# Optimization experiments

Measured on AMD Instinct MI355X. Metric: run time of the kernel, lower is better.

The kernel has to match this reference:

```python
import jax, jax.numpy as jnp
import numpy as np

IN_CH, D, K = 256, 128, 512

def setup_inputs() -> dict:
    key = jax.random.key(0)
    k1, k2, k3, k4 = jax.random.split(key, 4)
    x = jax.random.normal(k1, (16, IN_CH, 64, 64), dtype=jnp.float32)
    W = jax.random.normal(k2, (D, IN_CH), dtype=jnp.float32) * (1.0 / np.sqrt(IN_CH))
    b = jax.random.normal(k3, (D,), dtype=jnp.float32) * 0.01
    prototypes = jax.random.normal(k4, (K, D), dtype=jnp.float32) * 0.02
    gamma = jnp.asarray(1.0, dtype=jnp.float32)
    return {"x": x, "W": W, "b": b, "prototypes": prototypes, "gamma": gamma}

def reference(x, W, b, prototypes, gamma):
    n, c, h, w = x.shape
    # 1x1 conv projection: [n,c,h,w] -> [n,h,w,d]
    q = jnp.einsum('nchw,dc->nhwd', x, W) + b
    q_flat = q.reshape(n * h * w, -1)                      # [T, d]
    q_norm2 = jnp.sum(q_flat * q_flat, axis=1, keepdims=True)   # [T, 1]
    p_norm2 = jnp.sum(prototypes * prototypes, axis=1)[None, :] # [1, K]
    dist2 = q_norm2 + p_norm2 - 2.0 * (q_flat @ prototypes.T)   # [T, K]
    weights = jax.nn.softmax(-jnp.abs(gamma) * dist2, axis=1)
    return weights.reshape(n, h, w, -1).transpose(0, 3, 1, 2)   # [n, K, h, w]
```

## Files before the change

kernel.cpp:

```cpp
#include <hip/hip_runtime.h>

#define HW 4096
#define NCH 256
#define DIM 128
#define NPROTO 512

typedef __attribute__((ext_vector_type(4))) float f32x4;
typedef __attribute__((ext_vector_type(8))) short s16x8;
typedef __attribute__((ext_vector_type(4))) short s16x4;
typedef __attribute__((ext_vector_type(2))) unsigned u32x2;

__device__ __forceinline__ unsigned short f2bf(float f) {
  union { float f; unsigned u; } v; v.f = f;
  unsigned r = v.u + 0x7fffu + ((v.u >> 16) & 1u);
  return (unsigned short)(r >> 16);
}

__global__ __launch_bounds__(256) void prep_kernel(const float* __restrict__ P,
                                                   const float* __restrict__ Wm,
                                                   unsigned short* __restrict__ Pr,
                                                   unsigned short* __restrict__ Wr,
                                                   float* __restrict__ pn2) {
  const int tid = threadIdx.x;
  if (blockIdx.x < 8) {
    const int n  = blockIdx.x * 64 + (tid >> 2);
    const int qt = tid & 3;
    const float* row = P + n * DIM + qt * 32;
    unsigned short* dst = Pr + ((size_t)qt * NPROTO + n) * 32;
    float ssq = 0.f;
#pragma unroll
    for (int u = 0; u < 8; ++u) {
      f32x4 v = *(const f32x4*)(row + 4 * u);
      ssq += v.x * v.x + v.y * v.y + v.z * v.z + v.w * v.w;
      dst[4 * u + 0] = f2bf(v.x);
      dst[4 * u + 1] = f2bf(v.y);
      dst[4 * u + 2] = f2bf(v.z);
      dst[4 * u + 3] = f2bf(v.w);
    }
    ssq += __shfl_xor(ssq, 1);
    ssq += __shfl_xor(ssq, 2);
    if (qt == 0) pn2[n] = ssq;
  } else {
#pragma unroll
    for (int it = 0; it < 2; ++it) {
      const int p  = (blockIdx.x - 8) * 256 + tid + 512 * it;
      const int d  = p >> 3;
      const int ch = p & 7;
      const float* src = Wm + d * NCH + 32 * ch;
      unsigned short* dst = Wr + ((size_t)ch * DIM + d) * 32;
#pragma unroll
      for (int u = 0; u < 8; ++u) {
        f32x4 v = *(const f32x4*)(src + 4 * u);
        dst[4 * u + 0] = f2bf(v.x);
        dst[4 * u + 1] = f2bf(v.y);
        dst[4 * u + 2] = f2bf(v.z);
        dst[4 * u + 3] = f2bf(v.w);
      }
    }
  }
}

__global__ __launch_bounds__(512) void fused_kernel(const float* __restrict__ x,
                                                    const unsigned short* __restrict__ Wr,
                                                    const float* __restrict__ bias,
                                                    const unsigned short* __restrict__ Pr,
                                                    const float* __restrict__ pn2,
                                                    const float* __restrict__ gptr,
                                                    float* __restrict__ out) {
  __shared__ __align__(16) char smem[25088];
  unsigned short* x_s = (unsigned short*)smem;
  unsigned short* q_s = (unsigned short*)(smem + 16384);
  float* red  = (float*)smem;
  float* rmx  = (float*)smem + 256;
  float* rinv = (float*)smem + 288;

  const int tid  = threadIdx.x;
  const int p0   = blockIdx.x * 32;
  const int nimg = p0 >> 12;
  const int hw0  = p0 & 4095;
  const int wave = tid >> 6, lane = tid & 63;
  const int l15 = lane & 15, l4 = lane >> 4;
  const float g = fabsf(gptr[0]);

  {
    const int f  = tid & 7;
    const int gg = (tid >> 3) & 31;
    const int h  = tid >> 8;
    const float* src = x + (size_t)nimg * NCH * HW + hw0
                         + (size_t)(8 * gg + 4 * h) * HW + 4 * f;
    f32x4 v0 = *(const f32x4*)(src);
    f32x4 v1 = *(const f32x4*)(src + HW);
    f32x4 v2 = *(const f32x4*)(src + 2 * HW);
    f32x4 v3 = *(const f32x4*)(src + 3 * HW);
#pragma unroll
    for (int j = 0; j < 4; ++j) {
      const int pix  = 4 * f + j;
      const int slot = (gg & 24) | ((gg ^ (pix >> 1)) & 7);
      u32x2 wv;
      wv.x = (unsigned)f2bf(v0[j]) | ((unsigned)f2bf(v1[j]) << 16);
      wv.y = (unsigned)f2bf(v2[j]) | ((unsigned)f2bf(v3[j]) << 16);
      *(u32x2*)(x_s + pix * 256 + slot * 8 + 4 * h) = wv;
    }
  }
  __syncthreads();

  {
    const int mtb  = (wave & 3) * 2;
    const int nt   = wave >> 2;
    const int pixb = 16 * nt + l15;
    f32x4 qa0 = {0.f, 0.f, 0.f, 0.f};
    f32x4 qa1 = {0.f, 0.f, 0.f, 0.f};
#pragma unroll
    for (int kc = 0; kc < 8; ++kc) {
      const int gb   = 4 * kc + l4;
      const int slot = (gb & 24) | ((gb ^ (pixb >> 1)) & 7);
      s16x8 xb = *(const s16x8*)(x_s + pixb * 256 + slot * 8);
      const unsigned short* wb = Wr + (size_t)(kc * DIM + l15) * 32 + 8 * l4;
      s16x8 w0 = *(const s16x8*)(wb + (size_t)(16 * mtb) * 32);
      s16x8 w1 = *(const s16x8*)(wb + (size_t)(16 * (mtb + 1)) * 32);
      qa0 = __builtin_amdgcn_mfma_f32_16x16x32_bf16(w0, xb, qa0, 0, 0, 0);
      qa1 = __builtin_amdgcn_mfma_f32_16x16x32_bf16(w1, xb, qa1, 0, 0, 0);
    }
#pragma unroll
    for (int mm = 0; mm < 2; ++mm) {
      const int d0 = 16 * (mtb + mm) + 4 * l4;
      f32x4 qa = mm ? qa1 : qa0;
      f32x4 bv = *(const f32x4*)(bias + d0);
      s16x4 o;
#pragma unroll
      for (int r = 0; r < 4; ++r) o[r] = (short)f2bf(qa[r] + bv[r]);
      *(s16x4*)(q_s + pixb * 136 + d0) = o;
    }
  }
  __syncthreads();

  f32x4 acc[2][4];
#pragma unroll
  for (int i = 0; i < 2; ++i)
#pragma unroll
    for (int j = 0; j < 4; ++j)
#pragma unroll
      for (int r = 0; r < 4; ++r) acc[i][j][r] = 0.f;

#pragma unroll
  for (int kc = 0; kc < 4; ++kc) {
    s16x8 afr[2];
#pragma unroll
    for (int i = 0; i < 2; ++i)
      afr[i] = *(const s16x8*)(q_s + (16 * i + l15) * 136 + 32 * kc + 8 * l4);
    const unsigned short* pb = Pr + (size_t)(kc * NPROTO + 64 * wave + l15) * 32 + 8 * l4;
#pragma unroll
    for (int j = 0; j < 4; ++j) {
      s16x8 bfr = *(const s16x8*)(pb + (size_t)(16 * j) * 32);
#pragma unroll
      for (int i = 0; i < 2; ++i)
        acc[i][j] = __builtin_amdgcn_mfma_f32_16x16x32_bf16(afr[i], bfr, acc[i][j], 0, 0, 0);
    }
  }

  float pnv[4];
#pragma unroll
  for (int j = 0; j < 4; ++j) pnv[j] = pn2[64 * wave + 16 * j + l15];

#pragma unroll
  for (int i = 0; i < 2; ++i)
#pragma unroll
    for (int r = 0; r < 4; ++r) {
      float m = -1e30f;
#pragma unroll
      for (int j = 0; j < 4; ++j) {
        float lv = g * (2.f * acc[i][j][r] - pnv[j]);
        acc[i][j][r] = lv;
        m = fmaxf(m, lv);
      }
#pragma unroll
      for (int s = 1; s < 16; s <<= 1) m = fmaxf(m, __shfl_xor(m, s));
      if (l15 == 0) red[wave * 32 + 16 * i + 4 * l4 + r] = m;
    }
  __syncthreads();
  if (tid < 32) {
    float M = red[tid];
#pragma unroll
    for (int w = 1; w < 8; ++w) M = fmaxf(M, red[w * 32 + tid]);
    rmx[tid] = M;
  }
  __syncthreads();

#pragma unroll
  for (int i = 0; i < 2; ++i)
#pragma unroll
    for (int r = 0; r < 4; ++r) {
      const float M = rmx[16 * i + 4 * l4 + r];
      float s = 0.f;
#pragma unroll
      for (int j = 0; j < 4; ++j) {
        float e = __expf(acc[i][j][r] - M);
        acc[i][j][r] = e;
        s += e;
      }
#pragma unroll
      for (int t = 1; t < 16; t <<= 1) s += __shfl_xor(s, t);
      if (l15 == 0) red[wave * 32 + 16 * i + 4 * l4 + r] = s;
    }
  __syncthreads();
  if (tid < 32) {
    float S = 0.f;
#pragma unroll
    for (int w = 0; w < 8; ++w) S += red[w * 32 + tid];
    rinv[tid] = 1.f / S;
  }
  __syncthreads();

  float inv[2][4];
#pragma unroll
  for (int i = 0; i < 2; ++i)
#pragma unroll
    for (int r = 0; r < 4; ++r) inv[i][r] = rinv[16 * i + 4 * l4 + r];

  const size_t outbase = (size_t)nimg * NPROTO * HW + hw0;
#pragma unroll
  for (int j = 0; j < 4; ++j) {
    float* op = out + outbase + (size_t)(64 * wave + 16 * j + l15) * HW + 4 * l4;
#pragma unroll
    for (int i = 0; i < 2; ++i) {
      f32x4 o;
#pragma unroll
      for (int r = 0; r < 4; ++r) o[r] = acc[i][j][r] * inv[i][r];
      *(f32x4*)(op + 16 * i) = o;
    }
  }
}

extern "C" void kernel_launch(void* const* d_in, const int* in_sizes, int n_in,
                              void* d_out, int out_size, void* d_ws, size_t ws_size,
                              hipStream_t stream) {
  const float* x     = (const float*)d_in[0];
  const float* Wm    = (const float*)d_in[1];
  const float* bias  = (const float*)d_in[2];
  const float* prot  = (const float*)d_in[3];
  const float* gamma = (const float*)d_in[4];
  float* out = (float*)d_out;

  unsigned short* P_ws  = (unsigned short*)d_ws;
  unsigned short* W_ws  = (unsigned short*)((char*)d_ws + 131072);
  float*          pn2_w = (float*)((char*)d_ws + 131072 + 65536);

  prep_kernel<<<10, 256, 0, stream>>>(prot, Wm, P_ws, W_ws, pn2_w);
  fused_kernel<<<2048, 512, 0, stream>>>(x, W_ws, bias, P_ws, pn2_w, gamma, out);
}
```

Baseline: 232.9 us.

## Restructure fused kernel: 64-pixel tiles, per-wave full softmax, prefetch next tile

```diff
diff --git a/kernel.cpp b/kernel.cpp
--- a/kernel.cpp
+++ b/kernel.cpp
@@ -1,14 +1,16 @@
 #include <hip/hip_runtime.h>
+#include <math.h>
 
 #define HW 4096
 #define NCH 256
 #define DIM 128
 #define NPROTO 512
+#define L2E 1.4426950408889634f
 
 typedef __attribute__((ext_vector_type(4))) float f32x4;
 typedef __attribute__((ext_vector_type(8))) short s16x8;
 typedef __attribute__((ext_vector_type(4))) short s16x4;
-typedef __attribute__((ext_vector_type(2))) unsigned u32x2;
+typedef __attribute__((ext_vector_type(4))) unsigned u32x4;
 
 __device__ __forceinline__ unsigned short f2bf(float f) {
   union { float f; unsigned u; } v; v.f = f;
@@ -18,9 +20,10 @@
 
 __global__ __launch_bounds__(256) void prep_kernel(const float* __restrict__ P,
                                                    const float* __restrict__ Wm,
+                                                   const float* __restrict__ gptr,
                                                    unsigned short* __restrict__ Pr,
                                                    unsigned short* __restrict__ Wr,
-                                                   float* __restrict__ pn2) {
+                                                   float* __restrict__ pn2s) {
   const int tid = threadIdx.x;
   if (blockIdx.x < 8) {
     const int n  = blockIdx.x * 64 + (tid >> 2);
@@ -39,7 +42,7 @@
     }
     ssq += __shfl_xor(ssq, 1);
     ssq += __shfl_xor(ssq, 2);
-    if (qt == 0) pn2[n] = ssq;
+    if (qt == 0) pn2s[n] = fabsf(gptr[0]) * L2E * ssq;
   } else {
 #pragma unroll
     for (int it = 0; it < 2; ++it) {
@@ -60,173 +63,180 @@
   }
 }
 
-__global__ __launch_bounds__(512) void fused_kernel(const float* __restrict__ x,
-                                                    const unsigned short* __restrict__ Wr,
-                                                    const float* __restrict__ bias,
-                                                    const unsigned short* __restrict__ Pr,
-                                                    const float* __restrict__ pn2,
-                                                    const float* __restrict__ gptr,
-                                                    float* __restrict__ out) {
-  __shared__ __align__(16) char smem[25088];
-  unsigned short* x_s = (unsigned short*)smem;
-  unsigned short* q_s = (unsigned short*)(smem + 16384);
-  float* red  = (float*)smem;
-  float* rmx  = (float*)smem + 256;
-  float* rinv = (float*)smem + 288;
+__device__ __forceinline__ void x_load(const float* __restrict__ xbase,
+                                       int fq, int cg, f32x4 xv[16]) {
+#pragma unroll
+  for (int p = 0; p < 16; ++p)
+    xv[p] = *(const f32x4*)(xbase + (size_t)(16 * cg + p) * HW + 4 * fq);
+}
+
+__device__ __forceinline__ void x_pack_write(unsigned short* __restrict__ x_s,
+                                             int fq, int cg, const f32x4 xv[16]) {
+#pragma unroll
+  for (int jj = 0; jj < 4; ++jj) {
+    const int pix = 4 * fq + jj;
+#pragma unroll
+    for (int h = 0; h < 2; ++h) {
+      const int g = 2 * cg + h;
+      const int slot = (g & 24) | ((g ^ pix ^ (pix >> 2)) & 7);
+      u32x4 wv;
+#pragma unroll
+      for (int u = 0; u < 4; ++u) {
+        const int p = 8 * h + 2 * u;
+        wv[u] = (unsigned)f2bf(xv[p][jj]) | ((unsigned)f2bf(xv[p + 1][jj]) << 16);
+      }
+      *(u32x4*)(x_s + pix * 256 + slot * 8) = wv;
+    }
+  }
+}
+
+__global__ __launch_bounds__(256, 2) void fused_kernel(const float* __restrict__ x,
+                                                       const unsigned short* __restrict__ Wr,
+                                                       const float* __restrict__ bias,
+                                                       const unsigned short* __restrict__ Pr,
+                                                       const float* __restrict__ pn2s,
+                                                       const float* __restrict__ gptr,
+                                                       float* __restrict__ out) {
+  __shared__ __align__(16) unsigned short x_s[64 * 256];
+  __shared__ __align__(16) unsigned short q_s[64 * 152];
 
   const int tid  = threadIdx.x;
-  const int p0   = blockIdx.x * 32;
-  const int nimg = p0 >> 12;
-  const int hw0  = p0 & 4095;
   const int wave = tid >> 6, lane = tid & 63;
   const int l15 = lane & 15, l4 = lane >> 4;
-  const float g = fabsf(gptr[0]);
+  const int fq = tid & 15, cg = tid >> 4;
+  const float g2 = 2.f * fabsf(gptr[0]) * L2E;
 
   {
-    const int f  = tid & 7;
-    const int gg = (tid >> 3) & 31;
-    const int h  = tid >> 8;
-    const float* src = x + (size_t)nimg * NCH * HW + hw0
-                         + (size_t)(8 * gg + 4 * h) * HW + 4 * f;
-    f32x4 v0 = *(const f32x4*)(src);
-    f32x4 v1 = *(const f32x4*)(src + HW);
-    f32x4 v2 = *(const f32x4*)(src + 2 * HW);
-    f32x4 v3 = *(const f32x4*)(src + 3 * HW);
-#pragma unroll
-    for (int j = 0; j < 4; ++j) {
-      const int pix  = 4 * f + j;
-      const int slot = (gg & 24) | ((gg ^ (pix >> 1)) & 7);
-      u32x2 wv;
-      wv.x = (unsigned)f2bf(v0[j]) | ((unsigned)f2bf(v1[j]) << 16);
-      wv.y = (unsigned)f2bf(v2[j]) | ((unsigned)f2bf(v3[j]) << 16);
-      *(u32x2*)(x_s + pix * 256 + slot * 8 + 4 * h) = wv;
-    }
+    const int p0 = blockIdx.x * 64;
+    const float* xbase = x + (size_t)(p0 >> 12) * NCH * HW + (p0 & 4095);
+    f32x4 xv[16];
+    x_load(xbase, fq, cg, xv);
+    x_pack_write(x_s, fq, cg, xv);
   }
   __syncthreads();
 
-  {
-    const int mtb  = (wave & 3) * 2;
-    const int nt   = wave >> 2;
-    const int pixb = 16 * nt + l15;
-    f32x4 qa0 = {0.f, 0.f, 0.f, 0.f};
-    f32x4 qa1 = {0.f, 0.f, 0.f, 0.f};
-#pragma unroll
-    for (int kc = 0; kc < 8; ++kc) {
-      const int gb   = 4 * kc + l4;
-      const int slot = (gb & 24) | ((gb ^ (pixb >> 1)) & 7);
-      s16x8 xb = *(const s16x8*)(x_s + pixb * 256 + slot * 8);
-      const unsigned short* wb = Wr + (size_t)(kc * DIM + l15) * 32 + 8 * l4;
-      s16x8 w0 = *(const s16x8*)(wb + (size_t)(16 * mtb) * 32);
-      s16x8 w1 = *(const s16x8*)(wb + (size_t)(16 * (mtb + 1)) * 32);
-      qa0 = __builtin_amdgcn_mfma_f32_16x16x32_bf16(w0, xb, qa0, 0, 0, 0);
-      qa1 = __builtin_amdgcn_mfma_f32_16x16x32_bf16(w1, xb, qa1, 0, 0, 0);
-    }
-#pragma unroll
-    for (int mm = 0; mm < 2; ++mm) {
-      const int d0 = 16 * (mtb + mm) + 4 * l4;
-      f32x4 qa = mm ? qa1 : qa0;
-      f32x4 bv = *(const f32x4*)(bias + d0);
-      s16x4 o;
-#pragma unroll
-      for (int r = 0; r < 4; ++r) o[r] = (short)f2bf(qa[r] + bv[r]);
-      *(s16x4*)(q_s + pixb * 136 + d0) = o;
-    }
-  }
-  __syncthreads();
-
-  f32x4 acc[2][4];
-#pragma unroll
-  for (int i = 0; i < 2; ++i)
-#pragma unroll
-    for (int j = 0; j < 4; ++j)
-#pragma unroll
-      for (int r = 0; r < 4; ++r) acc[i][j][r] = 0.f;
-
-#pragma unroll
-  for (int kc = 0; kc < 4; ++kc) {
-    s16x8 afr[2];
-#pragma unroll
-    for (int i = 0; i < 2; ++i)
-      afr[i] = *(const s16x8*)(q_s + (16 * i + l15) * 136 + 32 * kc + 8 * l4);
-    const unsigned short* pb = Pr + (size_t)(kc * NPROTO + 64 * wave + l15) * 32 + 8 * l4;
-#pragma unroll
-    for (int j = 0; j < 4; ++j) {
-      s16x8 bfr = *(const s16x8*)(pb + (size_t)(16 * j) * 32);
-#pragma unroll
-      for (int i = 0; i < 2; ++i)
-        acc[i][j] = __builtin_amdgcn_mfma_f32_16x16x32_bf16(afr[i], bfr, acc[i][j], 0, 0, 0);
-    }
-  }
-
-  float pnv[4];
-#pragma unroll
-  for (int j = 0; j < 4; ++j) pnv[j] = pn2[64 * wave + 16 * j + l15];
-
-#pragma unroll
-  for (int i = 0; i < 2; ++i)
-#pragma unroll
-    for (int r = 0; r < 4; ++r) {
-      float m = -1e30f;
-#pragma unroll
-      for (int j = 0; j < 4; ++j) {
-        float lv = g * (2.f * acc[i][j][r] - pnv[j]);
-        acc[i][j][r] = lv;
-        m = fmaxf(m, lv);
-      }
-#pragma unroll
-      for (int s = 1; s < 16; s <<= 1) m = fmaxf(m, __shfl_xor(m, s));
-      if (l15 == 0) red[wave * 32 + 16 * i + 4 * l4 + r] = m;
-    }
-  __syncthreads();
-  if (tid < 32) {
-    float M = red[tid];
-#pragma unroll
-    for (int w = 1; w < 8; ++w) M = fmaxf(M, red[w * 32 + tid]);
-    rmx[tid] = M;
-  }
-  __syncthreads();
-
-#pragma unroll
-  for (int i = 0; i < 2; ++i)
-#pragma unroll
-    for (int r = 0; r < 4; ++r) {
-      const float M = rmx[16 * i + 4 * l4 + r];
-      float s = 0.f;
-#pragma unroll
-      for (int j = 0; j < 4; ++j) {
-        float e = __expf(acc[i][j][r] - M);
-        acc[i][j][r] = e;
-        s += e;
-      }
-#pragma unroll
-      for (int t = 1; t < 16; t <<= 1) s += __shfl_xor(s, t);
-      if (l15 == 0) red[wave * 32 + 16 * i + 4 * l4 + r] = s;
-    }
-  __syncthreads();
-  if (tid < 32) {
-    float S = 0.f;
-#pragma unroll
-    for (int w = 0; w < 8; ++w) S += red[w * 32 + tid];
-    rinv[tid] = 1.f / S;
-  }
-  __syncthreads();
-
-  float inv[2][4];
-#pragma unroll
-  for (int i = 0; i < 2; ++i)
-#pragma unroll
-    for (int r = 0; r < 4; ++r) inv[i][r] = rinv[16 * i + 4 * l4 + r];
-
-  const size_t outbase = (size_t)nimg * NPROTO * HW + hw0;
-#pragma unroll
-  for (int j = 0; j < 4; ++j) {
-    float* op = out + outbase + (size_t)(64 * wave + 16 * j + l15) * HW + 4 * l4;
-#pragma unroll
-    for (int i = 0; i < 2; ++i) {
+#pragma unroll
+  for (int tt = 0; tt < 2; ++tt) {
+    const int tile = blockIdx.x + 512 * tt;
+    const int p0   = tile * 64;
+    const int nimg = p0 >> 12;
+    const int hw0  = p0 & 4095;
+
+    {
+      f32x4 qacc[2][4];
+#pragma unroll
+      for (int mm = 0; mm < 2; ++mm)
+#pragma unroll
+        for (int nt = 0; nt < 4; ++nt)
+#pragma unroll
+          for (int r = 0; r < 4; ++r) qacc[mm][nt][r] = 0.f;
+
+#pragma unroll
+      for (int kc = 0; kc < 8; ++kc) {
+        s16x8 xb[4];
+#pragma unroll
+        for (int nt = 0; nt < 4; ++nt) {
+          const int pix  = 16 * nt + l15;
+          const int gblk = 4 * kc + l4;
+          const int slot = (gblk & 24) | ((gblk ^ pix ^ (pix >> 2)) & 7);
+          xb[nt] = *(const s16x8*)(x_s + pix * 256 + slot * 8);
+        }
+#pragma unroll
+        for (int mm = 0; mm < 2; ++mm) {
+          s16x8 wfr = *(const s16x8*)(Wr + (size_t)(kc * DIM + 16 * (2 * wave + mm) + l15) * 32 + 8 * l4);
+#pragma unroll
+          for (int nt = 0; nt < 4; ++nt)
+            qacc[mm][nt] = __builtin_amdgcn_mfma_f32_16x16x32_bf16(wfr, xb[nt], qacc[mm][nt], 0, 0, 0);
+        }
+      }
+#pragma unroll
+      for (int mm = 0; mm < 2; ++mm) {
+        const int d0 = 16 * (2 * wave + mm) + 4 * l4;
+        f32x4 bv = *(const f32x4*)(bias + d0);
+#pragma unroll
+        for (int nt = 0; nt < 4; ++nt) {
+          const int pix = 16 * nt + l15;
+          s16x4 o;
+#pragma unroll
+          for (int r = 0; r < 4; ++r) o[r] = (short)f2bf(qacc[mm][nt][r] + bv[r]);
+          *(s16x4*)(q_s + pix * 152 + d0) = o;
+        }
+      }
+    }
+    __syncthreads();
+
+    s16x8 afr[4];
+#pragma unroll
+    for (int kc = 0; kc < 4; ++kc)
+      afr[kc] = *(const s16x8*)(q_s + (16 * wave + l15) * 152 + 32 * kc + 8 * l4);
+
+    f32x4 acc[32];
+#pragma unroll
+    for (int j = 0; j < 32; ++j)
+#pragma unroll
+      for (int r = 0; r < 4; ++r) acc[j][r] = 0.f;
+
+#pragma unroll
+    for (int kc = 0; kc < 4; ++kc) {
+      const unsigned short* pb = Pr + (size_t)(kc * NPROTO + l15) * 32 + 8 * l4;
+#pragma unroll
+      for (int j = 0; j < 32; ++j) {
+        s16x8 bfr = *(const s16x8*)(pb + (size_t)(16 * j) * 32);
+        acc[j] = __builtin_amdgcn_mfma_f32_16x16x32_bf16(afr[kc], bfr, acc[j], 0, 0, 0);
+      }
+    }
+
+    f32x4 xv[16];
+    if (tt == 0) {
+      const int pn = (blockIdx.x + 512) * 64;
+      const float* xbase = x + (size_t)(pn >> 12) * NCH * HW + (pn & 4095);
+      x_load(xbase, fq, cg, xv);
+    }
+
+#pragma unroll
+    for (int j = 0; j < 32; ++j) {
+      const float p2 = pn2s[16 * j + l15];
+#pragma unroll
+      for (int r = 0; r < 4; ++r) acc[j][r] = g2 * acc[j][r] - p2;
+    }
+    f32x4 mx = acc[0];
+#pragma unroll
+    for (int j = 1; j < 32; ++j)
+#pragma unroll
+      for (int r = 0; r < 4; ++r) mx[r] = fmaxf(mx[r], acc[j][r]);
+#pragma unroll
+    for (int s = 1; s < 16; s <<= 1)
+#pragma unroll
+      for (int r = 0; r < 4; ++r) mx[r] = fmaxf(mx[r], __shfl_xor(mx[r], s));
+    f32x4 sm = {0.f, 0.f, 0.f, 0.f};
+#pragma unroll
+    for (int j = 0; j < 32; ++j)
+#pragma unroll
+      for (int r = 0; r < 4; ++r) {
+        const float e = exp2f(acc[j][r] - mx[r]);
+        acc[j][r] = e;
+        sm[r] += e;
+      }
+#pragma unroll
+    for (int s = 1; s < 16; s <<= 1)
+#pragma unroll
+      for (int r = 0; r < 4; ++r) sm[r] += __shfl_xor(sm[r], s);
+    f32x4 inv;
+#pragma unroll
+    for (int r = 0; r < 4; ++r) inv[r] = 1.0f / sm[r];
+
+    const size_t ob = (size_t)nimg * NPROTO * HW + hw0 + 16 * wave + 4 * l4;
+#pragma unroll
+    for (int j = 0; j < 32; ++j) {
       f32x4 o;
 #pragma unroll
-      for (int r = 0; r < 4; ++r) o[r] = acc[i][j][r] * inv[i][r];
-      *(f32x4*)(op + 16 * i) = o;
+      for (int r = 0; r < 4; ++r) o[r] = acc[j][r] * inv[r];
+      __builtin_nontemporal_store(o, (f32x4*)(out + ob + (size_t)(16 * j + l15) * HW));
+    }
+
+    if (tt == 0) {
+      x_pack_write(x_s, fq, cg, xv);
+      __syncthreads();
     }
   }
 }
@@ -245,6 +255,6 @@
   unsigned short* W_ws  = (unsigned short*)((char*)d_ws + 131072);
   float*          pn2_w = (float*)((char*)d_ws + 131072 + 65536);
 
-  prep_kernel<<<10, 256, 0, stream>>>(prot, Wm, P_ws, W_ws, pn2_w);
-  fused_kernel<<<2048, 512, 0, stream>>>(x, W_ws, bias, P_ws, pn2_w, gamma, out);
-}
+  prep_kernel<<<10, 256, 0, stream>>>(prot, Wm, gamma, P_ws, W_ws, pn2_w);
+  fused_kernel<<<512, 256, 0, stream>>>(x, W_ws, bias, P_ws, pn2_w, gamma, out);
+}
```

New measurement: 267.9 us. +15.0%, slower.
